# Kernel optimization log

Hardware: AMD Instinct MI355X
Metric: run time of the kernel (lower is better)

The kernel has to match this reference:

```python
import jax, jax.numpy as jnp
import numpy as np

B, C, H, W = 16, 512, 32, 32
EPS = 1e-5

def setup_inputs() -> dict:
    key = jax.random.key(0)
    ks = jax.random.split(key, 7)
    s = 1.0 / np.sqrt(C)
    return {
        "x": jax.random.normal(ks[0], (B, C, H, W), dtype=jnp.float32),
        "norm_w": jnp.ones((C,), jnp.float32),
        "norm_b": jnp.zeros((C,), jnp.float32),
        "qkv_w": jax.random.normal(ks[1], (3 * C, C), dtype=jnp.float32) * s,
        "qkv_b": jax.random.normal(ks[2], (3 * C,), dtype=jnp.float32) * 0.01,
        "out_w": jax.random.normal(ks[3], (C, C), dtype=jnp.float32) * s,
        "out_b": jax.random.normal(ks[4], (C,), dtype=jnp.float32) * 0.01,
    }

def reference(x, norm_w, norm_b, qkv_w, qkv_b, out_w, out_b):
    b, c, h, w = x.shape
    # GroupNorm with num_groups=1: normalize over (C,H,W) per sample, per-channel affine
    mean = jnp.mean(x, axis=(1, 2, 3), keepdims=True)
    var = jnp.var(x, axis=(1, 2, 3), keepdims=True)
    xn = (x - mean) * jax.lax.rsqrt(var + EPS)
    xn = xn * norm_w[None, :, None, None] + norm_b[None, :, None, None]
    # 1x1 conv QKV: [b,3c,h,w]
    qkv = jnp.einsum('bchw,oc->bohw', xn, qkv_w) + qkv_b[None, :, None, None]
    q, k, v = jnp.split(qkv, 3, axis=1)
    n = h * w
    q = q.transpose(0, 2, 3, 1).reshape(b, n, c)   # [b, N, c]
    k = k.reshape(b, c, n)                          # [b, c, N]
    v = v.transpose(0, 2, 3, 1).reshape(b, n, c)   # [b, N, c]
    scores = jnp.einsum('bnc,bcm->bnm', q, k) * (c ** -0.5)  # [b, N, N]
    attn = jax.nn.softmax(scores, axis=-1)
    out = jnp.einsum('bnm,bmc->bnc', attn, v)       # [b, N, c]
    out = out.reshape(b, h, w, c).transpose(0, 3, 1, 2)
    out = jnp.einsum('bchw,oc->bohw', out, out_w) + out_b[None, :, None, None]
    return out + x
```

## Files before the change

### kernel.cpp

```cpp
#include <hip/hip_runtime.h>
#include <math.h>

#define BATCH 16
#define CH    512
#define NTOK  1024
#define CHW   (CH * NTOK)
#define EPSV  1e-5f

typedef __attribute__((ext_vector_type(8))) short bf16x8;
typedef __attribute__((ext_vector_type(4))) float f32x4;

__device__ __forceinline__ unsigned short f2bf(float f) {
    union { float f; unsigned u; } cv; cv.f = f;
    unsigned r = cv.u + 0x7FFFu + ((cv.u >> 16) & 1u);
    return (unsigned short)(r >> 16);
}
__device__ __forceinline__ float bf2f(unsigned short u) {
    union { unsigned u; float f; } cv; cv.u = ((unsigned)u) << 16;
    return cv.f;
}

__device__ __forceinline__ void async16(const unsigned short* g, unsigned short* l) {
    __builtin_amdgcn_global_load_lds(
        (const __attribute__((address_space(1))) void*)g,
        (__attribute__((address_space(3))) void*)l,
        16, 0, 0);
}


static const size_t OFF_WQKV = 256;
static const size_t OFF_OW   = OFF_WQKV + 1572864;
static const size_t OFF_XNT  = OFF_OW   + 524288;
static const size_t OFF_QT   = OFF_XNT  + 16777216;
static const size_t OFF_KT   = OFF_QT   + 16777216;
static const size_t OFF_V    = OFF_KT   + 16777216;
static const size_t OFF_OT   = OFF_V    + 16777216;

__global__ void k_zero_stats(float* ws) {
    if (threadIdx.x < 64) ws[threadIdx.x] = 0.0f;
}

__global__ __launch_bounds__(256) void k_stats_partial(const float* __restrict__ x, float* __restrict__ ws) {
    int blk   = blockIdx.x;
    int b     = blk >> 6;
    int chunk = blk & 63;
    const float4* xp = (const float4*)(x + (size_t)b * CHW + (size_t)chunk * 8192);
    int t = threadIdx.x;
    float s = 0.0f, ss = 0.0f;
#pragma unroll
    for (int j = 0; j < 8; j++) {
        float4 v = xp[t + j * 256];
        s  += v.x + v.y + v.z + v.w;
        ss += v.x * v.x + v.y * v.y + v.z * v.z + v.w * v.w;
    }
#pragma unroll
    for (int off = 32; off; off >>= 1) {
        s  += __shfl_xor(s, off, 64);
        ss += __shfl_xor(ss, off, 64);
    }
    __shared__ float ls[4], lss[4];
    int wave = t >> 6, lane = t & 63;
    if (lane == 0) { ls[wave] = s; lss[wave] = ss; }
    __syncthreads();
    if (t == 0) {
        atomicAdd(&ws[b], ls[0] + ls[1] + ls[2] + ls[3]);
        atomicAdd(&ws[16 + b], lss[0] + lss[1] + lss[2] + lss[3]);
    }
}

__global__ void k_stats_final(float* ws) {
    int b = threadIdx.x;
    if (b < 16) {
        float inv  = 1.0f / (float)CHW;
        float mean = ws[b] * inv;
        float var  = ws[16 + b] * inv - mean * mean;
        ws[32 + b] = mean;
        ws[48 + b] = rsqrtf(var + EPSV);
    }
}

__global__ __launch_bounds__(256) void k_cvt2(const float* __restrict__ wq, const float* __restrict__ wo,
                                              unsigned short* __restrict__ WQ, unsigned short* __restrict__ WO) {
    int i = blockIdx.x * 256 + threadIdx.x;
    const float* src; unsigned short* dst; int off;
    if (i < 196608) { src = wq; dst = WQ; off = i; }
    else            { src = wo; dst = WO; off = i - 196608; }
    float4 v = ((const float4*)src)[off];
    ushort4 o;
    o.x = f2bf(v.x); o.y = f2bf(v.y); o.z = f2bf(v.z); o.w = f2bf(v.w);
    ((ushort4*)dst)[off] = o;
}

__global__ __launch_bounds__(256) void k_xnt(const float* __restrict__ x,
                                             const float* __restrict__ nw,
                                             const float* __restrict__ nb,
                                             const float* __restrict__ ws,
                                             unsigned short* __restrict__ xnt) {
    __shared__ float ls[64][65];
    int b  = blockIdx.z;
    int c0 = blockIdx.y * 64;
    int n0 = blockIdx.x * 64;
    float mean = ws[32 + b], rstd = ws[48 + b];
    int t = threadIdx.x;
    int cl = t >> 4, n4 = t & 15;
    const float* xb = x + (size_t)b * CHW;
#pragma unroll
    for (int i = 0; i < 4; i++) {
        int c = c0 + cl + i * 16;
        float a  = rstd * nw[c];
        float bb = nb[c] - mean * a;
        float4 v = *(const float4*)(xb + (size_t)c * NTOK + n0 + n4 * 4);
        ls[cl + i * 16][n4 * 4 + 0] = v.x * a + bb;
        ls[cl + i * 16][n4 * 4 + 1] = v.y * a + bb;
        ls[cl + i * 16][n4 * 4 + 2] = v.z * a + bb;
        ls[cl + i * 16][n4 * 4 + 3] = v.w * a + bb;
    }
    __syncthreads();
    int nl = t >> 4, c4 = t & 15;
    unsigned short* dst = xnt + (size_t)b * NTOK * CH;
#pragma unroll
    for (int i = 0; i < 4; i++) {
        int n = n0 + nl + i * 16;
        ushort4 o;
        o.x = f2bf(ls[c4 * 4 + 0][nl + i * 16]);
        o.y = f2bf(ls[c4 * 4 + 1][nl + i * 16]);
        o.z = f2bf(ls[c4 * 4 + 2][nl + i * 16]);
        o.w = f2bf(ls[c4 * 4 + 3][nl + i * 16]);
        *(ushort4*)(dst + (size_t)n * CH + c0 + c4 * 4) = o;
    }
}

__device__ __forceinline__ void mfma_core2(const unsigned short* __restrict__ A, int lda,
                                           const unsigned short* __restrict__ B, int ldb,
                                           int K, int m0, int n0,
                                           unsigned short* sm,
                                           f32x4 acc[4][8]) {
    const int t = threadIdx.x;
    const int w = t >> 6, lane = t & 63;
    const int wm = (w & 1) * 64, wn = (w >> 1) * 128;
    const int r16 = lane & 15, quad = lane >> 4;
#pragma unroll
    for (int i = 0; i < 4; i++)
#pragma unroll
        for (int j = 0; j < 8; j++) acc[i][j] = (f32x4){0.f, 0.f, 0.f, 0.f};
    const int sr = lane >> 2;
    const int sk = (((lane & 3) ^ ((lane >> 3) & 3))) * 8;
    const int swz = ((quad ^ (r16 >> 1)) & 3) * 8;
    const unsigned short* gA0 = A + (size_t)(m0 + w * 32 + sr) * lda + sk;
    const unsigned short* gA1 = gA0 + (size_t)16 * lda;
    const unsigned short* gB0 = B + (size_t)(n0 + w * 64 + sr) * ldb + sk;
    const unsigned short* gB1 = gB0 + (size_t)16 * ldb;
    const unsigned short* gB2 = gB0 + (size_t)32 * ldb;
    const unsigned short* gB3 = gB0 + (size_t)48 * ldb;
    unsigned short* lA0 = sm + (w * 32) * 32;
    unsigned short* lA1 = sm + (w * 32 + 16) * 32;
    unsigned short* lB0 = sm + 8192 + (w * 64) * 32;
    unsigned short* lB1 = lB0 + 16 * 32;
    unsigned short* lB2 = lB0 + 32 * 32;
    unsigned short* lB3 = lB0 + 48 * 32;
    const int T = K >> 5;
    async16(gA0, lA0); async16(gA1, lA1);
    async16(gB0, lB0); async16(gB1, lB1); async16(gB2, lB2); async16(gB3, lB3);
    for (int tt = 0; tt < T; tt++) {
        __syncthreads();
        const int ab = (tt & 1) << 12;
        const int bb = (tt & 1) << 13;
        if (tt + 1 < T) {
            const int nab = ab ^ 4096, nbb = bb ^ 8192;
            const int ko = (tt + 1) << 5;
            async16(gA0 + ko, lA0 + nab); async16(gA1 + ko, lA1 + nab);
            async16(gB0 + ko, lB0 + nbb); async16(gB1 + ko, lB1 + nbb);
            async16(gB2 + ko, lB2 + nbb); async16(gB3 + ko, lB3 + nbb);
        }
        bf16x8 af[4], bfr[8];
#pragma unroll
        for (int i = 0; i < 4; i++) af[i]  = *(const bf16x8*)(sm + ab + (wm + i * 16 + r16) * 32 + swz);
#pragma unroll
        for (int j = 0; j < 8; j++) bfr[j] = *(const bf16x8*)(sm + 8192 + bb + (wn + j * 16 + r16) * 32 + swz);
#pragma unroll
        for (int i = 0; i < 4; i++)
#pragma unroll
            for (int j = 0; j < 8; j++)
                acc[i][j] = __builtin_amdgcn_mfma_f32_16x16x32_bf16(af[i], bfr[j], acc[i][j], 0, 0, 0);
    }
}

#define TS1 136
#define TS2 264

__global__ __launch_bounds__(256, 2) void k_gemm_qkv(const unsigned short* __restrict__ Wq,
                                                     const float* __restrict__ qb,
                                                     const unsigned short* __restrict__ XNT,
                                                     unsigned short* __restrict__ QT,
                                                     unsigned short* __restrict__ KT,
                                                     unsigned short* __restrict__ V) {
    __shared__ __align__(16) unsigned short smem[256 * TS1];
    const int b  = blockIdx.z;
    const int m0 = blockIdx.y * 128;
    const int n0 = blockIdx.x * 256;
    f32x4 acc[4][8];
    mfma_core2(Wq, CH, XNT + (size_t)b * NTOK * CH, CH, CH, m0, n0, smem, acc);
    const int t = threadIdx.x;
    const int w = t >> 6, lane = t & 63;
    const int wm = (w & 1) * 64, wn = (w >> 1) * 128;
    const int r16 = lane & 15, quad = lane >> 4;
    const int region = m0 >> 9;
    __syncthreads();
    if (region < 2) {
#pragma unroll
        for (int i = 0; i < 4; i++) {
            const int ol = wm + i * 16 + quad * 4;
            const int og = m0 + ol;
            const float b0 = qb[og], b1 = qb[og + 1], b2 = qb[og + 2], b3 = qb[og + 3];
#pragma unroll
            for (int j = 0; j < 8; j++) {
                const int nl = wn + j * 16 + r16;
                f32x4 a = acc[i][j];
                ushort4 pk;
                pk.x = f2bf(a[0] + b0); pk.y = f2bf(a[1] + b1);
                pk.z = f2bf(a[2] + b2); pk.w = f2bf(a[3] + b3);
                *(ushort4*)(smem + nl * TS1 + ol) = pk;
            }
        }
        __syncthreads();
        unsigned short* dst = ((region == 0) ? QT : KT) + (size_t)b * NTOK * CH + (size_t)n0 * CH + (m0 & 511);
#pragma unroll
        for (int p = 0; p < 32; p++) {
            const int row = (t >> 5) + p * 8;
            const int seg = (t & 31) * 4;
            *(ushort4*)(dst + (size_t)row * CH + seg) = *(const ushort4*)(smem + row * TS1 + seg);
        }
    } else {
#pragma unroll
        for (int i = 0; i < 4; i++) {
            const int ol = wm + i * 16 + quad * 4;
            const int og = m0 + ol;
#pragma unroll
            for (int j = 0; j < 8; j++) {
                const int nl = wn + j * 16 + r16;
                f32x4 a = acc[i][j];
#pragma unroll
                for (int r = 0; r < 4; r++)
                    smem[(ol + r) * TS2 + nl] = f2bf(a[r] + qb[og + r]);
            }
        }
        __syncthreads();
        unsigned short* dst = V + (size_t)b * CH * NTOK + (size_t)(m0 & 511) * NTOK + n0;
#pragma unroll
        for (int p = 0; p < 32; p++) {
            const int row = (t >> 5) + (p & 15) * 8;
            const int seg = (t & 31) * 4 + (p >> 4) * 128;
            *(ushort4*)(dst + (size_t)row * NTOK + seg) = *(const ushort4*)(smem + row * TS2 + seg);
        }
    }
}

__global__ __launch_bounds__(256, 1) void k_attn(const unsigned short* __restrict__ QT,
                                                 const unsigned short* __restrict__ KTg,
                                                 const unsigned short* __restrict__ Vg,
                                                 unsigned short* __restrict__ OT) {
    __shared__ __align__(16) unsigned short sm[70016];
    unsigned short* smK = sm;
    unsigned short* smV = sm + 32768;
    unsigned short* smP = sm + 65536;
    float* lsumLDS = (float*)(sm + 69888);

    const int bid = blockIdx.x;
    const int xcd = bid & 7, slot = bid >> 3;
    const int b   = xcd * 2 + (slot & 1);
    const int q0  = (slot >> 1) * 64;

    const int t = threadIdx.x;
    const int w = t >> 6, lane = t & 63;
    const int r16 = lane & 15, quad = lane >> 4;
    const int srow = lane >> 2;
    const int sc   = (((lane & 3) ^ ((lane >> 3) & 3))) * 8;
    const int swz  = ((quad ^ (r16 >> 1)) & 3) * 8;

    const unsigned short* Qb = QT  + (size_t)b * NTOK * CH;
    const unsigned short* Kb = KTg + (size_t)b * NTOK * CH;
    const unsigned short* Vb = Vg  + (size_t)b * CH * NTOK;

    bf16x8 qf[16];
    {
        const unsigned short* qrow = Qb + (size_t)(q0 + w * 16 + r16) * CH + quad * 8;
#pragma unroll
        for (int kc = 0; kc < 16; kc++)
            qf[kc] = *(const bf16x8*)(qrow + kc * 32);
    }

    f32x4 accO[32];
#pragma unroll
    for (int j = 0; j < 32; j++) accO[j] = (f32x4){0.f, 0.f, 0.f, 0.f};
    float lsum[4] = {0.f, 0.f, 0.f, 0.f};
    const float scale = 0.044194173824159216f;

#pragma unroll
    for (int kc = 0; kc < 16; kc++)
        async16(Kb + (size_t)(w * 16 + srow) * CH + kc * 32 + sc, smK + (w * 16 + kc) * 512);
    __syncthreads();

    for (int kt = 0; kt < 16; kt++) {
        {
            const unsigned short* vbase = Vb + (size_t)kt * 64;
#pragma unroll
            for (int cg = 0; cg < 8; cg++)
#pragma unroll
                for (int kk = 0; kk < 2; kk++)
                    async16(vbase + (size_t)(w * 128 + cg * 16 + srow) * NTOK + kk * 32 + sc,
                            smV + ((w * 8 + cg) * 2 + kk) * 512);
        }
        f32x4 accS[4];
#pragma unroll
        for (int j = 0; j < 4; j++) accS[j] = (f32x4){0.f, 0.f, 0.f, 0.f};
#pragma unroll
        for (int kc = 0; kc < 16; kc++) {
            bf16x8 q = qf[kc];
#pragma unroll
            for (int j = 0; j < 4; j++) {
                bf16x8 kf = *(const bf16x8*)(smK + (j * 16 + kc) * 512 + r16 * 32 + swz);
                accS[j] = __builtin_amdgcn_mfma_f32_16x16x32_bf16(q, kf, accS[j], 0, 0, 0);
            }
        }
#pragma unroll
        for (int j = 0; j < 4; j++) {
#pragma unroll
            for (int r = 0; r < 4; r++) {
                float e = __expf(accS[j][r] * scale);
                lsum[r] += e;
                smP[(w * 16 + quad * 4 + r) * 68 + j * 16 + r16] = f2bf(e);
            }
        }
        __syncthreads();
        if (kt < 15) {
            const unsigned short* kbase = Kb + (size_t)(kt + 1) * 64 * CH;
#pragma unroll
            for (int kc = 0; kc < 16; kc++)
                async16(kbase + (size_t)(w * 16 + srow) * CH + kc * 32 + sc, smK + (w * 16 + kc) * 512);
        }
        bf16x8 pf[4][2];
#pragma unroll
        for (int j = 0; j < 4; j++)
#pragma unroll
            for (int kk = 0; kk < 2; kk++)
                pf[j][kk] = *(const bf16x8*)(smP + (j * 16 + r16) * 68 + kk * 32 + quad * 8);
#pragma unroll
        for (int cj = 0; cj < 8; cj++) {
            bf16x8 vf0 = *(const bf16x8*)(smV + ((w * 8 + cj) * 2 + 0) * 512 + r16 * 32 + swz);
            bf16x8 vf1 = *(const bf16x8*)(smV + ((w * 8 + cj) * 2 + 1) * 512 + r16 * 32 + swz);
#pragma unroll
            for (int j = 0; j < 4; j++) {
                accO[j * 8 + cj] = __builtin_amdgcn_mfma_f32_16x16x32_bf16(pf[j][0], vf0, accO[j * 8 + cj], 0, 0, 0);
                accO[j * 8 + cj] = __builtin_amdgcn_mfma_f32_16x16x32_bf16(pf[j][1], vf1, accO[j * 8 + cj], 0, 0, 0);
            }
        }
        __syncthreads();
    }

#pragma unroll
    for (int r = 0; r < 4; r++) {
        float v = lsum[r];
        v += __shfl_xor(v, 1, 64);
        v += __shfl_xor(v, 2, 64);
        v += __shfl_xor(v, 4, 64);
        v += __shfl_xor(v, 8, 64);
        if (r16 == 0) lsumLDS[w * 16 + quad * 4 + r] = v;
    }
    __syncthreads();
#pragma unroll
    for (int j = 0; j < 4; j++) {
        float iv[4];
#pragma unroll
        for (int r = 0; r < 4; r++) iv[r] = 1.0f / lsumLDS[j * 16 + quad * 4 + r];
#pragma unroll
        for (int cj = 0; cj < 8; cj++) {
            f32x4 a = accO[j * 8 + cj];
#pragma unroll
            for (int r = 0; r < 4; r++)
                sm[(j * 16 + quad * 4 + r) * 520 + w * 128 + cj * 16 + r16] = f2bf(a[r] * iv[r]);
        }
    }
    __syncthreads();
    unsigned short* dst = OT + (size_t)b * NTOK * CH + (size_t)q0 * CH;
#pragma unroll
    for (int p = 0; p < 32; p++) {
        const int row = (t >> 7) + p * 2;
        const int seg = (t & 127) * 4;
        *(ushort4*)(dst + (size_t)row * CH + seg) = *(const ushort4*)(sm + row * 520 + seg);
    }
}

__global__ __launch_bounds__(256, 2) void k_gemm_out(const unsigned short* __restrict__ OW,
                                                     const float* __restrict__ ob,
                                                     const unsigned short* __restrict__ OT,
                                                     const float* __restrict__ x,
                                                     float* __restrict__ out) {
    __shared__ __align__(16) unsigned short smem[24576];
    const int b  = blockIdx.z;
    const int m0 = blockIdx.y * 128;
    const int n0 = blockIdx.x * 256;
    f32x4 acc[4][8];
    mfma_core2(OW, CH, OT + (size_t)b * NTOK * CH, CH, CH, m0, n0, smem, acc);
    const int t = threadIdx.x;
    const int w = t >> 6, lane = t & 63;
    const int wm = (w & 1) * 64, wn = (w >> 1) * 128;
    const int r16 = lane & 15, quad = lane >> 4;
#pragma unroll
    for (int i = 0; i < 4; i++) {
        const int o0g = m0 + wm + i * 16 + quad * 4;
#pragma unroll
        for (int j = 0; j < 8; j++) {
            const int col = n0 + wn + j * 16 + r16;
            f32x4 a = acc[i][j];
#pragma unroll
            for (int r = 0; r < 4; r++) {
                size_t idx = (size_t)b * CHW + (size_t)(o0g + r) * NTOK + col;
                out[idx] = a[r] + ob[o0g + r] + x[idx];
            }
        }
    }
}

extern "C" void kernel_launch(void* const* d_in, const int* in_sizes, int n_in,
                              void* d_out, int out_size, void* d_ws, size_t ws_size,
                              hipStream_t stream) {
    const float* x      = (const float*)d_in[0];
    const float* norm_w = (const float*)d_in[1];
    const float* norm_b = (const float*)d_in[2];
    const float* qkv_w  = (const float*)d_in[3];
    const float* qkv_b  = (const float*)d_in[4];
    const float* out_w  = (const float*)d_in[5];
    const float* out_b  = (const float*)d_in[6];
    float* out = (float*)d_out;
    char* wsb  = (char*)d_ws;

    float* stats = (float*)wsb;
    unsigned short* WQ  = (unsigned short*)(wsb + OFF_WQKV);
    unsigned short* OW  = (unsigned short*)(wsb + OFF_OW);
    unsigned short* XNT = (unsigned short*)(wsb + OFF_XNT);
    unsigned short* QT  = (unsigned short*)(wsb + OFF_QT);
    unsigned short* KT  = (unsigned short*)(wsb + OFF_KT);
    unsigned short* V   = (unsigned short*)(wsb + OFF_V);
    unsigned short* OT  = (unsigned short*)(wsb + OFF_OT);

    k_zero_stats<<<1, 64, 0, stream>>>(stats);
    k_stats_partial<<<BATCH * 64, 256, 0, stream>>>(x, stats);
    k_stats_final<<<1, 16, 0, stream>>>(stats);
    k_cvt2<<<1024, 256, 0, stream>>>(qkv_w, out_w, WQ, OW);
    k_xnt<<<dim3(NTOK / 64, CH / 64, BATCH), 256, 0, stream>>>(x, norm_w, norm_b, stats, XNT);
    k_gemm_qkv<<<dim3(NTOK / 256, 3 * CH / 128, BATCH), 256, 0, stream>>>(WQ, qkv_b, XNT, QT, KT, V);
    k_attn<<<256, 256, 0, stream>>>(QT, KT, V, OT);
    k_gemm_out<<<dim3(NTOK / 256, CH / 128, BATCH), 256, 0, stream>>>(OW, out_b, OT, x, out);
}
```

Baseline: 252.7 us.

## Double attention block to eight waves splitting keys and output channels

The attention kernel now launches 512 threads per block. Waves are arranged as 4 query groups by 2 key halves for the QK^T step, and as 8 output-channel slices for the PV step. This halves per-wave accumulator registers and doubles the waves available to hide latency, and the two partial row sums are combined through LDS at the end. Separately, the stats-zeroing kernel is merged into the weight conversion kernel to remove one launch. The trade-off is more block-wide synchronisation traffic and the same grid of 256 blocks.

```diff
diff --git a/kernel.cpp b/kernel.cpp
--- a/kernel.cpp
+++ b/kernel.cpp
@@ -35,10 +35,6 @@
 static const size_t OFF_KT   = OFF_QT   + 16777216;
 static const size_t OFF_V    = OFF_KT   + 16777216;
 static const size_t OFF_OT   = OFF_V    + 16777216;
-
-__global__ void k_zero_stats(float* ws) {
-    if (threadIdx.x < 64) ws[threadIdx.x] = 0.0f;
-}
 
 __global__ __launch_bounds__(256) void k_stats_partial(const float* __restrict__ x, float* __restrict__ ws) {
     int blk   = blockIdx.x;
@@ -80,7 +76,9 @@
 }
 
 __global__ __launch_bounds__(256) void k_cvt2(const float* __restrict__ wq, const float* __restrict__ wo,
-                                              unsigned short* __restrict__ WQ, unsigned short* __restrict__ WO) {
+                                              unsigned short* __restrict__ WQ, unsigned short* __restrict__ WO,
+                                              float* __restrict__ stats) {
+    if (blockIdx.x == 0 && threadIdx.x < 64) stats[threadIdx.x] = 0.0f;
     int i = blockIdx.x * 256 + threadIdx.x;
     const float* src; unsigned short* dst; int off;
     if (i < 196608) { src = wq; dst = WQ; off = i; }
@@ -255,15 +253,15 @@
     }
 }
 
-__global__ __launch_bounds__(256, 1) void k_attn(const unsigned short* __restrict__ QT,
+__global__ __launch_bounds__(512, 2) void k_attn(const unsigned short* __restrict__ QT,
                                                  const unsigned short* __restrict__ KTg,
                                                  const unsigned short* __restrict__ Vg,
                                                  unsigned short* __restrict__ OT) {
-    __shared__ __align__(16) unsigned short sm[70016];
+    __shared__ __align__(16) unsigned short sm[70400];
     unsigned short* smK = sm;
     unsigned short* smV = sm + 32768;
     unsigned short* smP = sm + 65536;
-    float* lsumLDS = (float*)(sm + 69888);
+    float* lsum2 = (float*)(sm + 69888);
 
     const int bid = blockIdx.x;
     const int xcd = bid & 7, slot = bid >> 3;
@@ -272,6 +270,7 @@
 
     const int t = threadIdx.x;
     const int w = t >> 6, lane = t & 63;
+    const int qg = w & 3, h = w >> 2;
     const int r16 = lane & 15, quad = lane >> 4;
     const int srow = lane >> 2;
     const int sc   = (((lane & 3) ^ ((lane >> 3) & 3))) * 8;
@@ -283,75 +282,82 @@
 
     bf16x8 qf[16];
     {
-        const unsigned short* qrow = Qb + (size_t)(q0 + w * 16 + r16) * CH + quad * 8;
+        const unsigned short* qrow = Qb + (size_t)(q0 + qg * 16 + r16) * CH + quad * 8;
 #pragma unroll
         for (int kc = 0; kc < 16; kc++)
             qf[kc] = *(const bf16x8*)(qrow + kc * 32);
     }
 
-    f32x4 accO[32];
-#pragma unroll
-    for (int j = 0; j < 32; j++) accO[j] = (f32x4){0.f, 0.f, 0.f, 0.f};
+    f32x4 accO[16];
+#pragma unroll
+    for (int j = 0; j < 16; j++) accO[j] = (f32x4){0.f, 0.f, 0.f, 0.f};
     float lsum[4] = {0.f, 0.f, 0.f, 0.f};
     const float scale = 0.044194173824159216f;
 
 #pragma unroll
-    for (int kc = 0; kc < 16; kc++)
-        async16(Kb + (size_t)(w * 16 + srow) * CH + kc * 32 + sc, smK + (w * 16 + kc) * 512);
+    for (int kc2 = 0; kc2 < 8; kc2++) {
+        const int kc = h * 8 + kc2;
+        async16(Kb + (size_t)(qg * 16 + srow) * CH + kc * 32 + sc, smK + (qg * 16 + kc) * 512);
+    }
     __syncthreads();
 
     for (int kt = 0; kt < 16; kt++) {
         {
             const unsigned short* vbase = Vb + (size_t)kt * 64;
 #pragma unroll
-            for (int cg = 0; cg < 8; cg++)
+            for (int cgi = 0; cgi < 4; cgi++) {
+                const int cg = w * 4 + cgi;
 #pragma unroll
                 for (int kk = 0; kk < 2; kk++)
-                    async16(vbase + (size_t)(w * 128 + cg * 16 + srow) * NTOK + kk * 32 + sc,
-                            smV + ((w * 8 + cg) * 2 + kk) * 512);
-        }
-        f32x4 accS[4];
-#pragma unroll
-        for (int j = 0; j < 4; j++) accS[j] = (f32x4){0.f, 0.f, 0.f, 0.f};
+                    async16(vbase + (size_t)(cg * 16 + srow) * NTOK + kk * 32 + sc,
+                            smV + (cg * 2 + kk) * 512);
+            }
+        }
+        f32x4 accS[2];
+        accS[0] = (f32x4){0.f, 0.f, 0.f, 0.f};
+        accS[1] = (f32x4){0.f, 0.f, 0.f, 0.f};
 #pragma unroll
         for (int kc = 0; kc < 16; kc++) {
             bf16x8 q = qf[kc];
 #pragma unroll
-            for (int j = 0; j < 4; j++) {
-                bf16x8 kf = *(const bf16x8*)(smK + (j * 16 + kc) * 512 + r16 * 32 + swz);
+            for (int j = 0; j < 2; j++) {
+                const int jj = h * 2 + j;
+                bf16x8 kf = *(const bf16x8*)(smK + (jj * 16 + kc) * 512 + r16 * 32 + swz);
                 accS[j] = __builtin_amdgcn_mfma_f32_16x16x32_bf16(q, kf, accS[j], 0, 0, 0);
             }
         }
 #pragma unroll
-        for (int j = 0; j < 4; j++) {
+        for (int j = 0; j < 2; j++) {
 #pragma unroll
             for (int r = 0; r < 4; r++) {
                 float e = __expf(accS[j][r] * scale);
                 lsum[r] += e;
-                smP[(w * 16 + quad * 4 + r) * 68 + j * 16 + r16] = f2bf(e);
+                smP[(qg * 16 + quad * 4 + r) * 68 + (h * 2 + j) * 16 + r16] = f2bf(e);
             }
         }
         __syncthreads();
         if (kt < 15) {
             const unsigned short* kbase = Kb + (size_t)(kt + 1) * 64 * CH;
 #pragma unroll
-            for (int kc = 0; kc < 16; kc++)
-                async16(kbase + (size_t)(w * 16 + srow) * CH + kc * 32 + sc, smK + (w * 16 + kc) * 512);
+            for (int kc2 = 0; kc2 < 8; kc2++) {
+                const int kc = h * 8 + kc2;
+                async16(kbase + (size_t)(qg * 16 + srow) * CH + kc * 32 + sc, smK + (qg * 16 + kc) * 512);
+            }
         }
         bf16x8 pf[4][2];
 #pragma unroll
-        for (int j = 0; j < 4; j++)
+        for (int qj = 0; qj < 4; qj++)
 #pragma unroll
             for (int kk = 0; kk < 2; kk++)
-                pf[j][kk] = *(const bf16x8*)(smP + (j * 16 + r16) * 68 + kk * 32 + quad * 8);
-#pragma unroll
-        for (int cj = 0; cj < 8; cj++) {
-            bf16x8 vf0 = *(const bf16x8*)(smV + ((w * 8 + cj) * 2 + 0) * 512 + r16 * 32 + swz);
-            bf16x8 vf1 = *(const bf16x8*)(smV + ((w * 8 + cj) * 2 + 1) * 512 + r16 * 32 + swz);
-#pragma unroll
-            for (int j = 0; j < 4; j++) {
-                accO[j * 8 + cj] = __builtin_amdgcn_mfma_f32_16x16x32_bf16(pf[j][0], vf0, accO[j * 8 + cj], 0, 0, 0);
-                accO[j * 8 + cj] = __builtin_amdgcn_mfma_f32_16x16x32_bf16(pf[j][1], vf1, accO[j * 8 + cj], 0, 0, 0);
+                pf[qj][kk] = *(const bf16x8*)(smP + (qj * 16 + r16) * 68 + kk * 32 + quad * 8);
+#pragma unroll
+        for (int cj = 0; cj < 4; cj++) {
+            bf16x8 vf0 = *(const bf16x8*)(smV + ((w * 4 + cj) * 2 + 0) * 512 + r16 * 32 + swz);
+            bf16x8 vf1 = *(const bf16x8*)(smV + ((w * 4 + cj) * 2 + 1) * 512 + r16 * 32 + swz);
+#pragma unroll
+            for (int qj = 0; qj < 4; qj++) {
+                accO[qj * 4 + cj] = __builtin_amdgcn_mfma_f32_16x16x32_bf16(pf[qj][0], vf0, accO[qj * 4 + cj], 0, 0, 0);
+                accO[qj * 4 + cj] = __builtin_amdgcn_mfma_f32_16x16x32_bf16(pf[qj][1], vf1, accO[qj * 4 + cj], 0, 0, 0);
             }
         }
         __syncthreads();
@@ -364,27 +370,30 @@
         v += __shfl_xor(v, 2, 64);
         v += __shfl_xor(v, 4, 64);
         v += __shfl_xor(v, 8, 64);
-        if (r16 == 0) lsumLDS[w * 16 + quad * 4 + r] = v;
-    }
-    __syncthreads();
-#pragma unroll
-    for (int j = 0; j < 4; j++) {
+        if (r16 == 0) lsum2[h * 64 + qg * 16 + quad * 4 + r] = v;
+    }
+    __syncthreads();
+#pragma unroll
+    for (int qj = 0; qj < 4; qj++) {
         float iv[4];
 #pragma unroll
-        for (int r = 0; r < 4; r++) iv[r] = 1.0f / lsumLDS[j * 16 + quad * 4 + r];
-#pragma unroll
-        for (int cj = 0; cj < 8; cj++) {
-            f32x4 a = accO[j * 8 + cj];
+        for (int r = 0; r < 4; r++) {
+            const int row = qj * 16 + quad * 4 + r;
+            iv[r] = 1.0f / (lsum2[row] + lsum2[64 + row]);
+        }
+#pragma unroll
+        for (int cj = 0; cj < 4; cj++) {
+            f32x4 a = accO[qj * 4 + cj];
 #pragma unroll
             for (int r = 0; r < 4; r++)
-                sm[(j * 16 + quad * 4 + r) * 520 + w * 128 + cj * 16 + r16] = f2bf(a[r] * iv[r]);
+                sm[(qj * 16 + quad * 4 + r) * 520 + w * 64 + cj * 16 + r16] = f2bf(a[r] * iv[r]);
         }
     }
     __syncthreads();
     unsigned short* dst = OT + (size_t)b * NTOK * CH + (size_t)q0 * CH;
 #pragma unroll
-    for (int p = 0; p < 32; p++) {
-        const int row = (t >> 7) + p * 2;
+    for (int p = 0; p < 16; p++) {
+        const int row = (t >> 7) + p * 4;
         const int seg = (t & 127) * 4;
         *(ushort4*)(dst + (size_t)row * CH + seg) = *(const ushort4*)(sm + row * 520 + seg);
     }
@@ -443,12 +452,11 @@
     unsigned short* V   = (unsigned short*)(wsb + OFF_V);
     unsigned short* OT  = (unsigned short*)(wsb + OFF_OT);
 
-    k_zero_stats<<<1, 64, 0, stream>>>(stats);
+    k_cvt2<<<1024, 256, 0, stream>>>(qkv_w, out_w, WQ, OW, stats);
     k_stats_partial<<<BATCH * 64, 256, 0, stream>>>(x, stats);
     k_stats_final<<<1, 16, 0, stream>>>(stats);
-    k_cvt2<<<1024, 256, 0, stream>>>(qkv_w, out_w, WQ, OW);
     k_xnt<<<dim3(NTOK / 64, CH / 64, BATCH), 256, 0, stream>>>(x, norm_w, norm_b, stats, XNT);
     k_gemm_qkv<<<dim3(NTOK / 256, 3 * CH / 128, BATCH), 256, 0, stream>>>(WQ, qkv_b, XNT, QT, KT, V);
-    k_attn<<<256, 256, 0, stream>>>(QT, KT, V, OT);
+    k_attn<<<256, 512, 0, stream>>>(QT, KT, V, OT);
     k_gemm_out<<<dim3(NTOK / 256, CH / 128, BATCH), 256, 0, stream>>>(OW, out_b, OT, x, out);
 }
```

Result: faster. 238.8 us (-5.5%).
